# Kernel tuning notes

Hardware: AMD Instinct MI355X
Metric: run time of the kernel (lower is better)

## Reference

```python
import jax, jax.numpy as jnp
import numpy as np
import math

B, S, D = 2, 2048, 512
H = 8
DEPTH = D // H
MAX_REL = 1024
NEG_INF = -1.0e9


def skew(t):
    # t: (..., r, c). Pad a zero column on the left, reshape to move relative
    # logits into their absolute positions (Music Transformer skew trick).
    r, c = t.shape[-2], t.shape[-1]
    padded = jnp.pad(t, [(0, 0)] * (t.ndim - 1) + [(1, 0)])
    s = padded.reshape(-1, c + 1, r)[:, 1:]
    return s.reshape(t.shape)


def setup_inputs() -> dict:
    key = jax.random.key(0)
    ks = jax.random.split(key, 12)
    sc = 1.0 / math.sqrt(D)
    return {
        "q": jax.random.normal(ks[0], (B, S, D), jnp.float32),
        "k": jax.random.normal(ks[1], (B, S, D), jnp.float32),
        "v": jax.random.normal(ks[2], (B, S, D), jnp.float32),
        "mask": jax.random.randint(ks[3], (B, 1, S, S), 0, 2, jnp.int32),
        "Wq_w": jax.random.normal(ks[4], (D, D), jnp.float32) * sc,
        "Wq_b": jnp.zeros((D,), jnp.float32),
        "Wk_w": jax.random.normal(ks[5], (D, D), jnp.float32) * sc,
        "Wk_b": jnp.zeros((D,), jnp.float32),
        "Wv_w": jax.random.normal(ks[6], (D, D), jnp.float32) * sc,
        "Wv_b": jnp.zeros((D,), jnp.float32),
        "E": jax.random.normal(ks[7], (MAX_REL, D), jnp.float32),
        "Wo_w": jax.random.normal(ks[8], (D, D), jnp.float32) * sc,
        "Wo_b": jnp.zeros((D,), jnp.float32),
    }


def reference(q, k, v, mask, Wq_w, Wq_b, Wk_w, Wk_b, Wv_w, Wv_b, E, Wo_w, Wo_b):
    # Linear projections (torch Linear: x @ W^T + b)
    qp = q @ Wq_w.T + Wq_b
    kp = k @ Wk_w.T + Wk_b
    vp = v @ Wv_w.T + Wv_b

    # Required relative position embeddings for seq_len S (S >= MAX_REL here:
    # repeat E[0] for the first S-MAX_REL positions, then the full table).
    n_rep = max(0, S - MAX_REL)
    e = jnp.concatenate([jnp.tile(E[0:1], (n_rep, 1)), E[max(0, MAX_REL - S):]], axis=0)  # (S, D)

    # Split heads: (B,S,D)->(B,H,S,depth); e: (S,D)->(H,S,depth)
    qh = qp.reshape(B, S, H, DEPTH).transpose(0, 2, 1, 3)
    kh = kp.reshape(B, S, H, DEPTH).transpose(0, 2, 1, 3)
    vh = vp.reshape(B, S, H, DEPTH).transpose(0, 2, 1, 3)
    eh = e.reshape(S, H, DEPTH).transpose(1, 0, 2)

    QKt = jnp.einsum('bhqd,bhkd->bhqk', qh, kh)
    Srel = skew(jnp.einsum('bhqd,hkd->bhqk', qh, eh))
    logits = (QKt + Srel) / math.sqrt(DEPTH)
    logits = logits + mask.astype(logits.dtype) * NEG_INF
    attn = jnp.einsum('bhqk,bhkd->bhqd', jax.nn.softmax(logits, axis=-1), vh)

    # Merge heads and output projection
    out = attn.transpose(0, 2, 1, 3).reshape(B, S, D)
    return out @ Wo_w.T + Wo_b
```

## Files before the change

### kernel.cpp

```cpp
#include <hip/hip_runtime.h>
#include <hip/hip_bf16.h>

#define BB 2
#define SS 2048
#define DD 512
#define HH 8
#define DP 64
#define MR 1024

typedef __attribute__((ext_vector_type(8))) short bf16x8;
typedef __attribute__((ext_vector_type(4))) float floatx4;

static __device__ __forceinline__ unsigned short f2b(float x) {
    __hip_bfloat16 h = __float2bfloat16(x);
    return *reinterpret_cast<unsigned short*>(&h);
}
static __device__ __forceinline__ float b2f(unsigned short u) {
    __hip_bfloat16 h = *reinterpret_cast<__hip_bfloat16*>(&u);
    return __bfloat162float(h);
}
static __device__ __forceinline__ void gll16(const void* g, void* l) {
    __builtin_amdgcn_global_load_lds(
        (const __attribute__((address_space(1))) void*)g,
        (__attribute__((address_space(3))) void*)l, 16, 0, 0);
}
static __device__ __forceinline__ int xoff(int ks, int quad, int row) {
    return (((ks * 4 + quad) ^ (row & 7)) * 16);
}

__global__ __launch_bounds__(256) void prep_kernel(
    const float* __restrict__ Wq, const float* __restrict__ Wk,
    const float* __restrict__ Wv, const float* __restrict__ Wo,
    const float* __restrict__ E,  const float* __restrict__ q,
    const float* __restrict__ k,  const float* __restrict__ v,
    const int* __restrict__ mask,
    unsigned short* __restrict__ Wqb, unsigned short* __restrict__ Wkb,
    unsigned short* __restrict__ Wvb, unsigned short* __restrict__ Wob,
    unsigned short* __restrict__ Eb,  unsigned short* __restrict__ qb16,
    unsigned short* __restrict__ kb16, unsigned short* __restrict__ vb16,
    unsigned long long* __restrict__ bits)
{
    const int blk = blockIdx.x;
    if (blk < 7680) {
        const int gid = blk * 256 + threadIdx.x;
        const float* src; unsigned short* dst; int off;
        if      (gid < 65536)   { src = Wq; dst = Wqb;  off = gid; }
        else if (gid < 131072)  { src = Wk; dst = Wkb;  off = gid - 65536; }
        else if (gid < 196608)  { src = Wv; dst = Wvb;  off = gid - 131072; }
        else if (gid < 262144)  { src = Wo; dst = Wob;  off = gid - 196608; }
        else if (gid < 393216)  { src = E;  dst = Eb;   off = gid - 262144; }
        else if (gid < 917504)  { src = q;  dst = qb16; off = gid - 393216; }
        else if (gid < 1441792) { src = k;  dst = kb16; off = gid - 917504; }
        else                    { src = v;  dst = vb16; off = gid - 1441792; }
        float4 x = ((const float4*)src)[off];
        ushort4 u; u.x = f2b(x.x); u.y = f2b(x.y); u.z = f2b(x.z); u.w = f2b(x.w);
        ((ushort4*)dst)[off] = u;
    } else {
        const size_t wid = (size_t)(blk - 7680) * 4 + (threadIdx.x >> 6);
        const int lane = threadIdx.x & 63;
        const int mv = mask[wid * 64 + lane];
        unsigned long long bal = __ballot(mv != 0);
        if (lane == 0) bits[wid] = bal;
    }
}

__global__ __launch_bounds__(256) void gemm_proj(
    const unsigned short* __restrict__ Xq, const unsigned short* __restrict__ Xk,
    const unsigned short* __restrict__ Xv,
    const unsigned short* __restrict__ Wqb, const unsigned short* __restrict__ Wkb,
    const unsigned short* __restrict__ Wvb,
    const float* __restrict__ bq, const float* __restrict__ bk,
    const float* __restrict__ bv,
    unsigned short* __restrict__ qp, unsigned short* __restrict__ kp,
    unsigned short* __restrict__ vpT)
{
    const int z = blockIdx.z;
    const unsigned short* A  = (z == 0) ? Xq : (z == 1) ? Xk : Xv;
    const unsigned short* Wb = (z == 0) ? Wqb : (z == 1) ? Wkb : Wvb;
    const float* bias        = (z == 0) ? bq : (z == 1) ? bk : bv;

    __shared__ __align__(16) char parena[12288];
    char* AsB = parena;
    char* WsB = parena + 4096;
    const int t = threadIdx.x, lane = t & 63, w = t >> 6;
    const int quad = lane >> 4, l15 = lane & 15;
    const int wm = w >> 1, wn = w & 1;
    const int m0 = blockIdx.x * 32, n0 = blockIdx.y * 64;

    const int pa = w * 64 + lane;
    const int arow = pa >> 3, acol = (pa & 7) ^ (arow & 7);
    int wrow[2], wcol[2];
#pragma unroll
    for (int i = 0; i < 2; i++) {
        const int c = w * 2 + i;
        const int p = c * 64 + lane;
        wrow[i] = p >> 3; wcol[i] = (p & 7) ^ (wrow[i] & 7);
    }

    floatx4 acc[2];
    acc[0] = (floatx4){0.f, 0.f, 0.f, 0.f};
    acc[1] = (floatx4){0.f, 0.f, 0.f, 0.f};

    for (int k0 = 0; k0 < 512; k0 += 64) {
        if (k0) __syncthreads();
        gll16(A + (size_t)(m0 + arow) * 512 + k0 + acol * 8, AsB + w * 1024);
#pragma unroll
        for (int i = 0; i < 2; i++)
            gll16(Wb + (size_t)(n0 + wrow[i]) * 512 + k0 + wcol[i] * 8,
                  WsB + (w * 2 + i) * 1024);
        __syncthreads();
#pragma unroll
        for (int ks = 0; ks < 2; ks++) {
            bf16x8 a0 = *(const bf16x8*)(AsB + (wm * 16 + l15) * 128 + xoff(ks, quad, l15));
            bf16x8 b0 = *(const bf16x8*)(WsB + (wn * 32 + l15) * 128 + xoff(ks, quad, l15));
            bf16x8 b1 = *(const bf16x8*)(WsB + (wn * 32 + 16 + l15) * 128 + xoff(ks, quad, l15));
            acc[0] = __builtin_amdgcn_mfma_f32_16x16x32_bf16(a0, b0, acc[0], 0, 0, 0);
            acc[1] = __builtin_amdgcn_mfma_f32_16x16x32_bf16(a0, b1, acc[1], 0, 0, 0);
        }
    }

    if (z < 2) {
        unsigned short* Out = (z == 0) ? qp : kp;
#pragma unroll
        for (int ct = 0; ct < 2; ct++) {
            const int n = n0 + wn * 32 + ct * 16 + l15;
            const float bvl = bias[n];
#pragma unroll
            for (int r = 0; r < 4; r++) {
                const size_t m = (size_t)(m0 + wm * 16 + quad * 4 + r);
                Out[m * 512 + n] = f2b(acc[ct][r] + bvl);
            }
        }
    } else {
        __syncthreads();
        unsigned short* Ls = (unsigned short*)parena;
#pragma unroll
        for (int ct = 0; ct < 2; ct++) {
            const int dcol = wn * 32 + ct * 16 + l15;
            const float bvl = bias[n0 + dcol];
#pragma unroll
            for (int r = 0; r < 4; r++) {
                const int srow = wm * 16 + quad * 4 + r;
                Ls[dcol * 40 + srow] = f2b(acc[ct][r] + bvl);
            }
        }
        __syncthreads();
        const int bb = blockIdx.x >> 6, s0 = (blockIdx.x & 63) * 32, hh = blockIdx.y;
        const int drow = t >> 2, sc8 = (t & 3) * 8;
        *(uint4*)&vpT[((size_t)(bb * 8 + hh) * 64 + drow) * SS + s0 + sc8] =
            *(const uint4*)&Ls[drow * 40 + sc8];
    }
}

__global__ __launch_bounds__(256) void gemm_out(
    const unsigned short* __restrict__ A, const unsigned short* __restrict__ Wb,
    const float* __restrict__ bias, float* __restrict__ Out)
{
    __shared__ __align__(16) char parena[12288];
    char* AsB = parena;
    char* WsB = parena + 4096;
    const int t = threadIdx.x, lane = t & 63, w = t >> 6;
    const int quad = lane >> 4, l15 = lane & 15;
    const int wm = w >> 1, wn = w & 1;
    const int m0 = blockIdx.x * 32, n0 = blockIdx.y * 64;

    const int pa = w * 64 + lane;
    const int arow = pa >> 3, acol = (pa & 7) ^ (arow & 7);
    int wrow[2], wcol[2];
#pragma unroll
    for (int i = 0; i < 2; i++) {
        const int c = w * 2 + i;
        const int p = c * 64 + lane;
        wrow[i] = p >> 3; wcol[i] = (p & 7) ^ (wrow[i] & 7);
    }

    floatx4 acc[2];
    acc[0] = (floatx4){0.f, 0.f, 0.f, 0.f};
    acc[1] = (floatx4){0.f, 0.f, 0.f, 0.f};

    for (int k0 = 0; k0 < 512; k0 += 64) {
        if (k0) __syncthreads();
        gll16(A + (size_t)(m0 + arow) * 512 + k0 + acol * 8, AsB + w * 1024);
#pragma unroll
        for (int i = 0; i < 2; i++)
            gll16(Wb + (size_t)(n0 + wrow[i]) * 512 + k0 + wcol[i] * 8,
                  WsB + (w * 2 + i) * 1024);
        __syncthreads();
#pragma unroll
        for (int ks = 0; ks < 2; ks++) {
            bf16x8 a0 = *(const bf16x8*)(AsB + (wm * 16 + l15) * 128 + xoff(ks, quad, l15));
            bf16x8 b0 = *(const bf16x8*)(WsB + (wn * 32 + l15) * 128 + xoff(ks, quad, l15));
            bf16x8 b1 = *(const bf16x8*)(WsB + (wn * 32 + 16 + l15) * 128 + xoff(ks, quad, l15));
            acc[0] = __builtin_amdgcn_mfma_f32_16x16x32_bf16(a0, b0, acc[0], 0, 0, 0);
            acc[1] = __builtin_amdgcn_mfma_f32_16x16x32_bf16(a0, b1, acc[1], 0, 0, 0);
        }
    }
#pragma unroll
    for (int ct = 0; ct < 2; ct++) {
        const int n = n0 + wn * 32 + ct * 16 + l15;
        const float bvl = bias[n];
#pragma unroll
        for (int r = 0; r < 4; r++) {
            const size_t m = (size_t)(m0 + wm * 16 + quad * 4 + r);
            Out[m * 512 + n] = acc[ct][r] + bvl;
        }
    }
}

__global__ __launch_bounds__(256) void relg_kernel(
    const unsigned short* __restrict__ qp, const unsigned short* __restrict__ Eb,
    unsigned short* __restrict__ G)
{
    __shared__ unsigned short Ls[64 * 72];
    const int t = threadIdx.x, lane = t & 63, w = t >> 6;
    const int quad = lane >> 4, l15 = lane & 15;
    const int bh = blockIdx.z, b = bh >> 3, h = bh & 7;
    const int i0b = blockIdx.x * 64, t0 = blockIdx.y * 64;

    const unsigned short* Ar = qp + ((size_t)b * SS + i0b + w * 16 + l15) * DD + h * DP;
    bf16x8 a0 = *(const bf16x8*)(Ar + quad * 8);
    bf16x8 a1 = *(const bf16x8*)(Ar + 32 + quad * 8);

    floatx4 acc[4];
#pragma unroll
    for (int ct = 0; ct < 4; ct++) acc[ct] = (floatx4){0.f, 0.f, 0.f, 0.f};
#pragma unroll
    for (int ct = 0; ct < 4; ct++) {
        const unsigned short* Br = Eb + (size_t)(t0 + ct * 16 + l15) * DD + h * DP;
        bf16x8 b0 = *(const bf16x8*)(Br + quad * 8);
        bf16x8 b1 = *(const bf16x8*)(Br + 32 + quad * 8);
        acc[ct] = __builtin_amdgcn_mfma_f32_16x16x32_bf16(a0, b0, acc[ct], 0, 0, 0);
        acc[ct] = __builtin_amdgcn_mfma_f32_16x16x32_bf16(a1, b1, acc[ct], 0, 0, 0);
    }
#pragma unroll
    for (int ct = 0; ct < 4; ct++)
#pragma unroll
        for (int r = 0; r < 4; r++)
            Ls[(w * 16 + quad * 4 + r) * 72 + ct * 16 + l15] = f2b(acc[ct][r]);
    __syncthreads();
#pragma unroll
    for (int p = 0; p < 2; p++) {
        const int idx = p * 256 + t;
        const int row = idx >> 3, c8 = (idx & 7) * 8;
        *(uint4*)&G[((size_t)bh * SS + i0b + row) * MR + t0 + c8] =
            *(const uint4*)&Ls[row * 72 + c8];
    }
}

static __device__ __forceinline__ void load_rel(
    const unsigned short* __restrict__ pdiag, int i0w, int gi, int k0,
    float d0a, float d0b, int quad, float relv[2][4])
{
#pragma unroll
    for (int ct = 0; ct < 2; ct++) {
        const int k0c = k0 + ct * 16;
        const int gj0 = k0c + quad * 4;
        const int dmax = i0w + 15 - k0c;
        const int dmin = i0w - (k0c + 15);
        if (dmin >= MR) {
#pragma unroll
            for (int r = 0; r < 4; r++) relv[ct][r] = d0a;
        } else if (dmin >= 0 && dmax <= MR - 1) {
#pragma unroll
            for (int r = 0; r < 4; r++) relv[ct][r] = b2f(pdiag[1023 + gj0 + r]);
        } else if (dmax <= -2 && dmin >= -(MR + 1)) {
#pragma unroll
            for (int r = 0; r < 4; r++) relv[ct][r] = d0b;
        } else if (dmax <= -(MR + 2)) {
#pragma unroll
            for (int r = 0; r < 4; r++) relv[ct][r] = b2f(pdiag[gj0 - 2 + r]);
        } else {
#pragma unroll
            for (int r = 0; r < 4; r++) {
                const int gj = gj0 + r;
                const int dd = gi - gj;
                float rl;
                if (dd >= MR) rl = d0a;
                else if (dd >= 0) rl = b2f(pdiag[1023 + gj]);
                else if (dd == -1) rl = 0.0f;
                else if (dd >= -(MR + 1)) rl = d0b;
                else rl = b2f(pdiag[gj - 2]);
                relv[ct][r] = rl;
            }
        }
    }
}

__global__ __launch_bounds__(256, 4) void attn_kernel(
    const unsigned short* __restrict__ qp, const unsigned short* __restrict__ kp,
    const unsigned short* __restrict__ vpT, const unsigned int* __restrict__ mb32,
    const unsigned short* __restrict__ G, unsigned short* __restrict__ ao)
{
    __shared__ __align__(16) char smem[38016];
    const int t = threadIdx.x, lane = t & 63, w = t >> 6;
    const int quad = lane >> 4, l15 = lane & 15;
    const int wr = w >> 1, kh = w & 1;
    const int bh = blockIdx.y, b = bh >> 3, h = bh & 7;
    const int i0w = blockIdx.x * 32 + wr * 16;
    const int gi = i0w + l15;

    const unsigned short* kb = kp + (size_t)b * SS * DD + h * DP;
    const unsigned short* vb = vpT + (size_t)bh * DP * SS;
    const unsigned short* Gb = G + (size_t)bh * SS * MR;
    const unsigned int* mrow32 = mb32 + ((size_t)b * SS + gi) * 64;

    const unsigned short* qrow = qp + ((size_t)b * SS + gi) * DD + h * DP;
    bf16x8 qf0 = *(const bf16x8*)(qrow + quad * 8);
    bf16x8 qf1 = *(const bf16x8*)(qrow + 32 + quad * 8);

    const unsigned short* pdiag = Gb + (size_t)gi * 1023;
    const float d0a = b2f(Gb[(size_t)gi * MR]);
    const float d0b = b2f(Gb[(size_t)min(gi + 1, SS - 1) * MR]);

    char* Kh = smem + kh * 8192;
    char* Vh = smem + 16384 + kh * 8192;
    char* Pt = smem + 32768 + w * 1280;

    int kofs[2], vofs[2], dst[2];
#pragma unroll
    for (int i = 0; i < 2; i++) {
        const int c = wr * 2 + i;
        const int p = c * 64 + lane;
        const int krow = p >> 3, kcol = (p & 7) ^ (krow & 7);
        kofs[i] = krow * DD + kcol * 8;
        const int vrow = p >> 2, vcol = (p & 3) ^ (vrow & 3);
        vofs[i] = vrow * SS + vcol * 8;
        dst[i] = c * 1024;
    }

    floatx4 oacc[4];
#pragma unroll
    for (int ct = 0; ct < 4; ct++) oacc[ct] = (floatx4){0.f, 0.f, 0.f, 0.f};
    float lsum = 0.0f;

    {
        const int k0 = kh * 1024;
        gll16(kb + (size_t)k0 * DD + kofs[0], Kh + dst[0]);
        gll16(kb + (size_t)k0 * DD + kofs[1], Kh + dst[1]);
        gll16(vb + k0 + vofs[0], Vh + dst[0]);
        gll16(vb + k0 + vofs[1], Vh + dst[1]);
    }
    unsigned int mwv = mrow32[kh * 32];
    float relv[2][4];
    load_rel(pdiag, i0w, gi, kh * 1024, d0a, d0b, quad, relv);

    for (int it = 0; it < 32; it++) {
        const int cur = it & 1;
        __syncthreads();
        if (it + 1 < 32) {
            const int k0n = kh * 1024 + (it + 1) * 32;
            const int nb = (cur ^ 1) * 4096;
            gll16(kb + (size_t)k0n * DD + kofs[0], Kh + nb + dst[0]);
            gll16(kb + (size_t)k0n * DD + kofs[1], Kh + nb + dst[1]);
            gll16(vb + k0n + vofs[0], Vh + nb + dst[0]);
            gll16(vb + k0n + vofs[1], Vh + nb + dst[1]);
        }
        const unsigned int mcur = mwv;
        float relc[2][4];
#pragma unroll
        for (int ct = 0; ct < 2; ct++)
#pragma unroll
            for (int r = 0; r < 4; r++) relc[ct][r] = relv[ct][r];

        char* Kc = Kh + cur * 4096;
        char* Vc = Vh + cur * 4096;

        floatx4 acc[2];
#pragma unroll
        for (int ct = 0; ct < 2; ct++) {
            const unsigned int nib = (mcur >> (ct * 16 + quad * 4)) & 0xFu;
            floatx4 a;
#pragma unroll
            for (int r = 0; r < 4; r++)
                a[r] = relc[ct][r] + (((nib >> r) & 1u) ? -8.0e9f : 0.0f);
            const int row = ct * 16 + l15;
            bf16x8 kf0 = *(const bf16x8*)(Kc + row * 128 + ((quad ^ (l15 & 7)) * 16));
            bf16x8 kf1 = *(const bf16x8*)(Kc + row * 128 + (((4 + quad) ^ (l15 & 7)) * 16));
            a = __builtin_amdgcn_mfma_f32_16x16x32_bf16(kf0, qf0, a, 0, 0, 0);
            a = __builtin_amdgcn_mfma_f32_16x16x32_bf16(kf1, qf1, a, 0, 0, 0);
            acc[ct] = a;
        }

        {
            const int itn = (it + 1 < 32) ? it + 1 : 31;
            mwv = mrow32[kh * 32 + itn];
            load_rel(pdiag, i0w, gi, kh * 1024 + itn * 32, d0a, d0b, quad, relv);
        }

#pragma unroll
        for (int ct = 0; ct < 2; ct++) {
            const float p0 = __expf(acc[ct][0] * 0.125f - 18.75f);
            const float p1 = __expf(acc[ct][1] * 0.125f - 18.75f);
            const float p2 = __expf(acc[ct][2] * 0.125f - 18.75f);
            const float p3 = __expf(acc[ct][3] * 0.125f - 18.75f);
            lsum += (p0 + p1) + (p2 + p3);
            ushort4 u;
            u.x = f2b(p0); u.y = f2b(p1); u.z = f2b(p2); u.w = f2b(p3);
            *(ushort4*)(Pt + l15 * 80 + ct * 32 + quad * 8) = u;
        }

        bf16x8 pt = *(const bf16x8*)(Pt + l15 * 80 + quad * 16);
#pragma unroll
        for (int ct = 0; ct < 4; ct++) {
            const int drow = ct * 16 + l15;
            bf16x8 vf = *(const bf16x8*)(Vc + drow * 64 + ((quad ^ (drow & 3)) * 16));
            oacc[ct] = __builtin_amdgcn_mfma_f32_16x16x32_bf16(vf, pt, oacc[ct], 0, 0, 0);
        }
    }

    lsum += __shfl_xor(lsum, 16);
    lsum += __shfl_xor(lsum, 32);

    __syncthreads();
    float* OmW = (float*)(smem + wr * 4352);
    float* MlW = (float*)(smem + 37888);
    if (kh == 1) {
#pragma unroll
        for (int ct = 0; ct < 4; ct++)
            *(floatx4*)&OmW[l15 * 68 + ct * 16 + quad * 4] = oacc[ct];
        if (lane < 16) MlW[wr * 16 + lane] = lsum;
    }
    __syncthreads();
    if (kh == 0) {
        const float inv = 1.0f / (lsum + MlW[wr * 16 + l15]);
#pragma unroll
        for (int ct = 0; ct < 4; ct++) {
            floatx4 o1 = *(const floatx4*)&OmW[l15 * 68 + ct * 16 + quad * 4];
            ushort4 u;
            u.x = f2b((oacc[ct][0] + o1[0]) * inv);
            u.y = f2b((oacc[ct][1] + o1[1]) * inv);
            u.z = f2b((oacc[ct][2] + o1[2]) * inv);
            u.w = f2b((oacc[ct][3] + o1[3]) * inv);
            *(ushort4*)&ao[((size_t)b * SS + gi) * DD + h * DP + ct * 16 + quad * 4] = u;
        }
    }
}

extern "C" void kernel_launch(void* const* d_in, const int* in_sizes, int n_in,
                              void* d_out, int out_size, void* d_ws, size_t ws_size,
                              hipStream_t stream)
{
    const float* q    = (const float*)d_in[0];
    const float* k    = (const float*)d_in[1];
    const float* v    = (const float*)d_in[2];
    const int*   mask = (const int*)d_in[3];
    const float* Wq_w = (const float*)d_in[4];
    const float* Wq_b = (const float*)d_in[5];
    const float* Wk_w = (const float*)d_in[6];
    const float* Wk_b = (const float*)d_in[7];
    const float* Wv_w = (const float*)d_in[8];
    const float* Wv_b = (const float*)d_in[9];
    const float* E    = (const float*)d_in[10];
    const float* Wo_w = (const float*)d_in[11];
    const float* Wo_b = (const float*)d_in[12];
    float* out = (float*)d_out;

    char* ws = (char*)d_ws;
    unsigned short* G    = (unsigned short*)ws;
    unsigned short* qp   = (unsigned short*)(ws + 67108864);
    unsigned short* kp   = qp + 2097152;
    unsigned short* vpT  = kp + 2 * 2097152;
    unsigned short* qb16 = vpT + 2097152;
    unsigned short* kb16 = qb16 + 2097152;
    unsigned short* vb16 = kb16 + 2097152;
    unsigned short* aob  = qb16;
    unsigned long long* mbits = (unsigned long long*)(ws + 67108864 + 7 * 4194304);
    unsigned short* Wqb = (unsigned short*)(ws + 67108864 + 7 * 4194304 + 1048576);
    unsigned short* Wkb = Wqb + 262144;
    unsigned short* Wvb = Wkb + 262144;
    unsigned short* Wob = Wvb + 262144;
    unsigned short* Ebf = Wob + 262144;

    dim3 blk(256);
    hipLaunchKernelGGL(prep_kernel, dim3(40448), blk, 0, stream,
                       Wq_w, Wk_w, Wv_w, Wo_w, E, q, k, v, mask,
                       Wqb, Wkb, Wvb, Wob, Ebf, qb16, kb16, vb16, mbits);
    hipLaunchKernelGGL(gemm_proj, dim3(128, 8, 3), blk, 0, stream,
                       qb16, kb16, vb16, Wqb, Wkb, Wvb, Wq_b, Wk_b, Wv_b,
                       qp, kp, vpT);
    hipLaunchKernelGGL(relg_kernel, dim3(32, 16, 16), blk, 0, stream, qp, Ebf, G);
    hipLaunchKernelGGL(attn_kernel, dim3(64, 16), blk, 0, stream,
                       qp, kp, vpT, (const unsigned int*)mbits, G, aob);
    hipLaunchKernelGGL(gemm_out, dim3(128, 8), blk, 0, stream, aob, Wob, Wo_b, out);
}
```

Baseline: 254.7 us.

## Prefetch raw relative logits early and hoist K/V LDS reads before MFMAs

Splits relative-logit loading into an issue step, which loads raw bf16 values one iteration ahead, and a convert step done just before use, so global load latency overlaps the previous iteration. All K and V fragments are read from LDS up front before the MFMA chains, and the MFMA sections are wrapped in s_setprio to favour matrix issue. This raises register pressure under a 4-wave-per-SIMD launch bound and may cause spills.

```diff
diff --git a/kernel.cpp b/kernel.cpp
--- a/kernel.cpp
+++ b/kernel.cpp
@@ -247,9 +247,11 @@
     }
 }
 
-static __device__ __forceinline__ void load_rel(
-    const unsigned short* __restrict__ pdiag, int i0w, int gi, int k0,
-    float d0a, float d0b, int quad, float relv[2][4])
+struct RelPF { ushort4 hi; ushort4 lo; int path; };
+
+static __device__ __forceinline__ void rel_issue(
+    const unsigned short* __restrict__ pdiag, int i0w, int k0, int quad,
+    RelPF pf[2])
 {
 #pragma unroll
     for (int ct = 0; ct < 2; ct++) {
@@ -257,31 +259,55 @@
         const int gj0 = k0c + quad * 4;
         const int dmax = i0w + 15 - k0c;
         const int dmin = i0w - (k0c + 15);
-        if (dmin >= MR) {
-#pragma unroll
-            for (int r = 0; r < 4; r++) relv[ct][r] = d0a;
-        } else if (dmin >= 0 && dmax <= MR - 1) {
-#pragma unroll
-            for (int r = 0; r < 4; r++) relv[ct][r] = b2f(pdiag[1023 + gj0 + r]);
-        } else if (dmax <= -2 && dmin >= -(MR + 1)) {
-#pragma unroll
-            for (int r = 0; r < 4; r++) relv[ct][r] = d0b;
-        } else if (dmax <= -(MR + 2)) {
-#pragma unroll
-            for (int r = 0; r < 4; r++) relv[ct][r] = b2f(pdiag[gj0 - 2 + r]);
-        } else {
-#pragma unroll
-            for (int r = 0; r < 4; r++) {
-                const int gj = gj0 + r;
-                const int dd = gi - gj;
-                float rl;
-                if (dd >= MR) rl = d0a;
-                else if (dd >= 0) rl = b2f(pdiag[1023 + gj]);
-                else if (dd == -1) rl = 0.0f;
-                else if (dd >= -(MR + 1)) rl = d0b;
-                else rl = b2f(pdiag[gj - 2]);
-                relv[ct][r] = rl;
-            }
+        int path;
+        if (dmin >= MR) path = 0;
+        else if (dmin >= 0 && dmax <= MR - 1) path = 1;
+        else if (dmax <= -2 && dmin >= -(MR + 1)) path = 2;
+        else if (dmax <= -(MR + 2)) path = 3;
+        else path = 4;
+        pf[ct].path = path;
+        if (path == 1 || path == 4) {
+            const unsigned short* p = pdiag + 1023 + gj0;
+            pf[ct].hi.x = p[0]; pf[ct].hi.y = p[1];
+            pf[ct].hi.z = p[2]; pf[ct].hi.w = p[3];
+        }
+        if (path == 3 || path == 4) {
+            const unsigned short* p = pdiag + max(gj0 - 2, 0);
+            pf[ct].lo.x = p[0]; pf[ct].lo.y = p[1];
+            pf[ct].lo.z = p[2]; pf[ct].lo.w = p[3];
+        }
+    }
+}
+
+static __device__ __forceinline__ void rel_convert(
+    const RelPF& pf, int gi, int k0c, int quad,
+    float d0a, float d0b, float relc[4])
+{
+    const int path = pf.path;
+    if (path == 0) {
+        relc[0] = relc[1] = relc[2] = relc[3] = d0a;
+    } else if (path == 1) {
+        relc[0] = b2f(pf.hi.x); relc[1] = b2f(pf.hi.y);
+        relc[2] = b2f(pf.hi.z); relc[3] = b2f(pf.hi.w);
+    } else if (path == 2) {
+        relc[0] = relc[1] = relc[2] = relc[3] = d0b;
+    } else if (path == 3) {
+        relc[0] = b2f(pf.lo.x); relc[1] = b2f(pf.lo.y);
+        relc[2] = b2f(pf.lo.z); relc[3] = b2f(pf.lo.w);
+    } else {
+        const int gj0 = k0c + quad * 4;
+        const unsigned short hv[4] = {pf.hi.x, pf.hi.y, pf.hi.z, pf.hi.w};
+        const unsigned short lv[4] = {pf.lo.x, pf.lo.y, pf.lo.z, pf.lo.w};
+#pragma unroll
+        for (int r = 0; r < 4; r++) {
+            const int dd = gi - (gj0 + r);
+            float rl;
+            if (dd >= MR) rl = d0a;
+            else if (dd >= 0) rl = b2f(hv[r]);
+            else if (dd == -1) rl = 0.0f;
+            else if (dd >= -(MR + 1)) rl = d0b;
+            else rl = b2f(lv[r]);
+            relc[r] = rl;
         }
     }
 }
@@ -341,8 +367,8 @@
         gll16(vb + k0 + vofs[1], Vh + dst[1]);
     }
     unsigned int mwv = mrow32[kh * 32];
-    float relv[2][4];
-    load_rel(pdiag, i0w, gi, kh * 1024, d0a, d0b, quad, relv);
+    RelPF pf[2];
+    rel_issue(pdiag, i0w, kh * 1024, quad, pf);
 
     for (int it = 0; it < 32; it++) {
         const int cur = it & 1;
@@ -356,14 +382,33 @@
             gll16(vb + k0n + vofs[1], Vh + nb + dst[1]);
         }
         const unsigned int mcur = mwv;
+
         float relc[2][4];
-#pragma unroll
-        for (int ct = 0; ct < 2; ct++)
-#pragma unroll
-            for (int r = 0; r < 4; r++) relc[ct][r] = relv[ct][r];
+        rel_convert(pf[0], gi, kh * 1024 + it * 32,      quad, d0a, d0b, relc[0]);
+        rel_convert(pf[1], gi, kh * 1024 + it * 32 + 16, quad, d0a, d0b, relc[1]);
+
+        {
+            const int itn = (it + 1 < 32) ? it + 1 : 31;
+            mwv = mrow32[kh * 32 + itn];
+            rel_issue(pdiag, i0w, kh * 1024 + itn * 32, quad, pf);
+        }
 
         char* Kc = Kh + cur * 4096;
         char* Vc = Vh + cur * 4096;
+
+        bf16x8 kf[2][2];
+#pragma unroll
+        for (int ct = 0; ct < 2; ct++) {
+            const int row = ct * 16 + l15;
+            kf[ct][0] = *(const bf16x8*)(Kc + row * 128 + ((quad ^ (l15 & 7)) * 16));
+            kf[ct][1] = *(const bf16x8*)(Kc + row * 128 + (((4 + quad) ^ (l15 & 7)) * 16));
+        }
+        bf16x8 vf[4];
+#pragma unroll
+        for (int ct = 0; ct < 4; ct++) {
+            const int drow = ct * 16 + l15;
+            vf[ct] = *(const bf16x8*)(Vc + drow * 64 + ((quad ^ (drow & 3)) * 16));
+        }
 
         floatx4 acc[2];
 #pragma unroll
@@ -373,19 +418,15 @@
 #pragma unroll
             for (int r = 0; r < 4; r++)
                 a[r] = relc[ct][r] + (((nib >> r) & 1u) ? -8.0e9f : 0.0f);
-            const int row = ct * 16 + l15;
-            bf16x8 kf0 = *(const bf16x8*)(Kc + row * 128 + ((quad ^ (l15 & 7)) * 16));
-            bf16x8 kf1 = *(const bf16x8*)(Kc + row * 128 + (((4 + quad) ^ (l15 & 7)) * 16));
-            a = __builtin_amdgcn_mfma_f32_16x16x32_bf16(kf0, qf0, a, 0, 0, 0);
-            a = __builtin_amdgcn_mfma_f32_16x16x32_bf16(kf1, qf1, a, 0, 0, 0);
             acc[ct] = a;
         }
-
-        {
-            const int itn = (it + 1 < 32) ? it + 1 : 31;
-            mwv = mrow32[kh * 32 + itn];
-            load_rel(pdiag, i0w, gi, kh * 1024 + itn * 32, d0a, d0b, quad, relv);
-        }
+        __builtin_amdgcn_s_setprio(1);
+#pragma unroll
+        for (int ct = 0; ct < 2; ct++) {
+            acc[ct] = __builtin_amdgcn_mfma_f32_16x16x32_bf16(kf[ct][0], qf0, acc[ct], 0, 0, 0);
+            acc[ct] = __builtin_amdgcn_mfma_f32_16x16x32_bf16(kf[ct][1], qf1, acc[ct], 0, 0, 0);
+        }
+        __builtin_amdgcn_s_setprio(0);
 
 #pragma unroll
         for (int ct = 0; ct < 2; ct++) {
@@ -400,12 +441,11 @@
         }
 
         bf16x8 pt = *(const bf16x8*)(Pt + l15 * 80 + quad * 16);
-#pragma unroll
-        for (int ct = 0; ct < 4; ct++) {
-            const int drow = ct * 16 + l15;
-            bf16x8 vf = *(const bf16x8*)(Vc + drow * 64 + ((quad ^ (drow & 3)) * 16));
-            oacc[ct] = __builtin_amdgcn_mfma_f32_16x16x32_bf16(vf, pt, oacc[ct], 0, 0, 0);
-        }
+        __builtin_amdgcn_s_setprio(1);
+#pragma unroll
+        for (int ct = 0; ct < 4; ct++)
+            oacc[ct] = __builtin_amdgcn_mfma_f32_16x16x32_bf16(vf[ct], pt, oacc[ct], 0, 0, 0);
+        __builtin_amdgcn_s_setprio(0);
     }
 
     lsum += __shfl_xor(lsum, 16);
```

Result: no change. 253.7 us (-0.4%).
